# Performance work log

Measured on AMD Instinct MI355X. Metric: run time of the kernel, lower is better.

## Reference

```python
import jax, jax.numpy as jnp
import numpy as np

B, N, D, K = 32, 1024, 768, 512

def setup_inputs() -> dict:
    key = jax.random.key(0)
    k1, k2 = jax.random.split(key)
    img_feat_map = jax.random.normal(k1, (B, N, D), dtype=jnp.float32)
    codebook = jax.random.normal(k2, (K, D), dtype=jnp.float32)
    return {"img_feat_map": img_feat_map, "codebook": codebook}

def reference(img_feat_map, codebook):
    # squared L2 distances between each token and each codebook vector
    x_sq = jnp.sum(img_feat_map ** 2, axis=2, keepdims=True)          # [B,N,1]
    c_sq = jnp.sum(codebook ** 2, axis=1)[None, None, :]              # [1,1,K]
    dot = jnp.einsum('bnd,kd->bnk', img_feat_map, codebook)           # [B,N,K]
    distances = x_sq + c_sq - 2.0 * dot                               # [B,N,K]
    soft_assignments = jax.nn.softmax(-distances, axis=2)             # [B,N,K]
    # aggregate tokens per codebook slot
    aggregated = jnp.einsum('bnk,bnd->bkd', soft_assignments, img_feat_map)  # [B,K,D]
    return aggregated
```

## Files before the change

### kernel.cpp

```cpp
#include <hip/hip_runtime.h>
#include <math.h>

#define BB 32
#define NN 1024
#define DD 768
#define KK 512
#define MM (BB * NN)

typedef _Float16 half8 __attribute__((ext_vector_type(8)));
typedef _Float16 half4 __attribute__((ext_vector_type(4)));
typedef float floatx4 __attribute__((ext_vector_type(4)));

__device__ __forceinline__ void load_lds16(const void* g, void* l) {
    __builtin_amdgcn_global_load_lds(
        (const __attribute__((address_space(1))) unsigned int*)g,
        (__attribute__((address_space(3))) unsigned int*)l, 16, 0, 0);
}

__global__ __launch_bounds__(256) void prep_codebook(const float* __restrict__ cb,
                                                     _Float16* __restrict__ Cbh,
                                                     float* __restrict__ csq) {
    int k = blockIdx.x;
    const float* row = cb + (size_t)k * DD;
    _Float16* orow = Cbh + (size_t)k * DD;
    float s = 0.f;
    for (int d = threadIdx.x; d < DD; d += 256) {
        float v = row[d];
        s += v * v;
        orow[d] = (_Float16)v;
    }
    #pragma unroll
    for (int off = 32; off > 0; off >>= 1) s += __shfl_down(s, off);
    __shared__ float sm[4];
    int lane = threadIdx.x & 63, wid = threadIdx.x >> 6;
    if (lane == 0) sm[wid] = s;
    __syncthreads();
    if (threadIdx.x == 0) csq[k] = sm[0] + sm[1] + sm[2] + sm[3];
}

__global__ __launch_bounds__(512, 4) void fused_logits_softmax(
    const float* __restrict__ X,
    const _Float16* __restrict__ Cbh,
    const float* __restrict__ csq,
    _Float16* __restrict__ St,
    _Float16* __restrict__ Xt)
{
    __shared__ _Float16 Cs[2][512][32];
    __shared__ _Float16 Xs[2][64][32];
    __shared__ float redbuf[8][64];
    __shared__ float gred[64];

    const int t = threadIdx.x;
    const int w = t >> 6;
    const int lane = t & 63;
    const int l15 = lane & 15;
    const int quad = lane >> 4;
    const int wk = w * 64;
    const int gm0 = blockIdx.x * 64;
    const int b = gm0 >> 10;
    const int n0 = gm0 & 1023;

    const int qs = (quad ^ ((l15 >> 1) & 3)) * 8;

    float cs[4];
    #pragma unroll
    for (int ki = 0; ki < 4; ki++) cs[ki] = csq[wk + ki * 16 + l15];

    floatx4 acc[4][4] = {};

    const int cr = t >> 2;
    const int cq = (t & 3) ^ ((t >> 3) & 3);
    const float* xsrc = X + (size_t)(gm0 + cr) * DD + cq * 8;

    const int tdr = t >> 4;
    const int tn4 = (t & 15) * 4;

    float4 xa, xb;
    if (t < 256) { xa = *(const float4*)xsrc; xb = *(const float4*)(xsrc + 4); }

    #pragma unroll
    for (int c = 0; c < 4; c++)
        load_lds16(Cbh + (size_t)(c * 128 + cr) * DD + cq * 8,
                   (_Float16*)Cs[0] + (c * 512 + t) * 8);
    if (t < 256) {
        half8 h;
        h[0] = (_Float16)xa.x; h[1] = (_Float16)xa.y; h[2] = (_Float16)xa.z; h[3] = (_Float16)xa.w;
        h[4] = (_Float16)xb.x; h[5] = (_Float16)xb.y; h[6] = (_Float16)xb.z; h[7] = (_Float16)xb.w;
        *(half8*)&Xs[0][cr][(t & 3) * 8] = h;
        xa = *(const float4*)(xsrc + 32);
        xb = *(const float4*)(xsrc + 36);
    }
    __syncthreads();

    int cur = 0;
    for (int it = 0; it < 24; ++it) {
        const int d0 = it * 32;
        if (it + 1 < 24) {
            const int d0n = d0 + 32;
            #pragma unroll
            for (int c = 0; c < 4; c++)
                load_lds16(Cbh + (size_t)(c * 128 + cr) * DD + d0n + cq * 8,
                           (_Float16*)Cs[cur ^ 1] + (c * 512 + t) * 8);
            asm volatile("" ::: "memory");
            if (t < 256) {
                half8 h;
                h[0] = (_Float16)xa.x; h[1] = (_Float16)xa.y; h[2] = (_Float16)xa.z; h[3] = (_Float16)xa.w;
                h[4] = (_Float16)xb.x; h[5] = (_Float16)xb.y; h[6] = (_Float16)xb.z; h[7] = (_Float16)xb.w;
                *(half8*)&Xs[cur ^ 1][cr][(t & 3) * 8] = h;
                if (it + 2 < 24) {
                    xa = *(const float4*)(xsrc + (it + 2) * 32);
                    xb = *(const float4*)(xsrc + (it + 2) * 32 + 4);
                }
            }
        }
        {
            half4 xo;
            #pragma unroll
            for (int j = 0; j < 4; j++) {
                int n = tn4 + j;
                xo[j] = *((const _Float16*)Xs[cur] + n * 32 +
                          (((tdr >> 3) ^ ((n >> 1) & 3)) << 3) + (tdr & 7));
            }
            *(half4*)&Xt[((size_t)b * DD + d0 + tdr) * NN + n0 + tn4] = xo;
        }
        half8 af[4], bf[4];
        #pragma unroll
        for (int mi = 0; mi < 4; mi++)
            af[mi] = *(half8*)((_Float16*)Xs[cur] + (mi * 16 + l15) * 32 + qs);
        #pragma unroll
        for (int ki = 0; ki < 4; ki++)
            bf[ki] = *(half8*)((_Float16*)Cs[cur] + (wk + ki * 16 + l15) * 32 + qs);
        #pragma unroll
        for (int mi = 0; mi < 4; mi++)
            #pragma unroll
            for (int ki = 0; ki < 4; ki++)
                acc[mi][ki] = __builtin_amdgcn_mfma_f32_16x16x32_f16(af[mi], bf[ki], acc[mi][ki], 0, 0, 0);
        if (it + 1 < 24) {
            if (it + 2 < 24 && w < 4)
                asm volatile("s_waitcnt vmcnt(3) lgkmcnt(0)" ::: "memory");
            else
                asm volatile("s_waitcnt vmcnt(1) lgkmcnt(0)" ::: "memory");
            __builtin_amdgcn_s_barrier();
            cur ^= 1;
        }
    }

    float pmax[4][4];
    #pragma unroll
    for (int mi = 0; mi < 4; mi++)
        #pragma unroll
        for (int r = 0; r < 4; r++) {
            float m = -1e30f;
            #pragma unroll
            for (int ki = 0; ki < 4; ki++)
                m = fmaxf(m, 2.f * acc[mi][ki][r] - cs[ki]);
            pmax[mi][r] = m;
        }
    #pragma unroll
    for (int off = 1; off < 16; off <<= 1)
        #pragma unroll
        for (int mi = 0; mi < 4; mi++)
            #pragma unroll
            for (int r = 0; r < 4; r++)
                pmax[mi][r] = fmaxf(pmax[mi][r], __shfl_xor(pmax[mi][r], off));
    if (l15 == 0) {
        #pragma unroll
        for (int mi = 0; mi < 4; mi++)
            #pragma unroll
            for (int r = 0; r < 4; r++)
                redbuf[w][mi * 16 + quad * 4 + r] = pmax[mi][r];
    }
    __syncthreads();
    if (t < 64) {
        float g = redbuf[0][t];
        #pragma unroll
        for (int wv = 1; wv < 8; wv++) g = fmaxf(g, redbuf[wv][t]);
        gred[t] = g;
    }
    __syncthreads();
    float gmax[4][4];
    #pragma unroll
    for (int mi = 0; mi < 4; mi++)
        #pragma unroll
        for (int r = 0; r < 4; r++)
            gmax[mi][r] = gred[mi * 16 + quad * 4 + r];
    __syncthreads();

    float psum[4][4] = {};
    #pragma unroll
    for (int mi = 0; mi < 4; mi++)
        #pragma unroll
        for (int ki = 0; ki < 4; ki++) {
            floatx4 e;
            #pragma unroll
            for (int r = 0; r < 4; r++) {
                e[r] = __expf(2.f * acc[mi][ki][r] - cs[ki] - gmax[mi][r]);
                psum[mi][r] += e[r];
            }
            acc[mi][ki] = e;
        }
    #pragma unroll
    for (int off = 1; off < 16; off <<= 1)
        #pragma unroll
        for (int mi = 0; mi < 4; mi++)
            #pragma unroll
            for (int r = 0; r < 4; r++)
                psum[mi][r] += __shfl_xor(psum[mi][r], off);
    if (l15 == 0) {
        #pragma unroll
        for (int mi = 0; mi < 4; mi++)
            #pragma unroll
            for (int r = 0; r < 4; r++)
                redbuf[w][mi * 16 + quad * 4 + r] = psum[mi][r];
    }
    __syncthreads();
    if (t < 64) {
        float s = redbuf[0][t];
        #pragma unroll
        for (int wv = 1; wv < 8; wv++) s += redbuf[wv][t];
        gred[t] = 1.f / s;
    }
    __syncthreads();
    float ginv[4][4];
    #pragma unroll
    for (int mi = 0; mi < 4; mi++)
        #pragma unroll
        for (int r = 0; r < 4; r++)
            ginv[mi][r] = gred[mi * 16 + quad * 4 + r];

    #pragma unroll
    for (int mi = 0; mi < 4; mi++)
        #pragma unroll
        for (int ki = 0; ki < 4; ki++) {
            half4 s4;
            #pragma unroll
            for (int r = 0; r < 4; r++)
                s4[r] = (_Float16)(acc[mi][ki][r] * ginv[mi][r]);
            int k = wk + ki * 16 + l15;
            *(half4*)&St[((size_t)b * KK + k) * NN + n0 + mi * 16 + quad * 4] = s4;
        }
}

__global__ __launch_bounds__(256, 4) void gemm2_mfma(const _Float16* __restrict__ St,
                                                     const _Float16* __restrict__ Xt,
                                                     float* __restrict__ out) {
    __shared__ _Float16 As[2][128][32];
    __shared__ _Float16 Bs[2][128][32];

    const int lin = blockIdx.x;
    const int wg = (lin & 7) * 96 + (lin >> 3);
    const int b = wg / 24;
    const int rr = wg % 24;
    const int k0 = (rr / 6) * 128;
    const int d0 = (rr % 6) * 128;

    const int t = threadIdx.x;
    const int wave = t >> 6;
    const int lane = t & 63;
    const int wm = (wave >> 1) * 64;
    const int wn = (wave & 1) * 64;
    const int l15 = lane & 15;
    const int quad = lane >> 4;
    const int qs = (quad ^ ((l15 >> 1) & 3)) * 8;

    const int cr = t >> 2;
    const int cq = (t & 3) ^ ((t >> 3) & 3);

    floatx4 acc[4][4] = {};

    const _Float16* Abase = St + ((size_t)b * KK + k0) * NN;
    const _Float16* Bbase = Xt + ((size_t)b * DD + d0) * NN;

    #pragma unroll
    for (int c = 0; c < 2; c++) {
        load_lds16(Abase + (size_t)(c * 64 + cr) * NN + cq * 8,
                   (_Float16*)As[0] + (c * 256 + t) * 8);
        load_lds16(Bbase + (size_t)(c * 64 + cr) * NN + cq * 8,
                   (_Float16*)Bs[0] + (c * 256 + t) * 8);
    }
    __syncthreads();

    int cur = 0;
    for (int it = 0; it < 32; ++it) {
        if (it + 1 < 32) {
            const int n0 = (it + 1) * 32;
            #pragma unroll
            for (int c = 0; c < 2; c++) {
                load_lds16(Abase + (size_t)(c * 64 + cr) * NN + n0 + cq * 8,
                           (_Float16*)As[cur ^ 1] + (c * 256 + t) * 8);
                load_lds16(Bbase + (size_t)(c * 64 + cr) * NN + n0 + cq * 8,
                           (_Float16*)Bs[cur ^ 1] + (c * 256 + t) * 8);
            }
        }
        half8 af[4], bf[4];
        #pragma unroll
        for (int i = 0; i < 4; i++) af[i] = *(half8*)&As[cur][wm + i * 16 + l15][qs];
        #pragma unroll
        for (int i = 0; i < 4; i++) bf[i] = *(half8*)&Bs[cur][wn + i * 16 + l15][qs];
        #pragma unroll
        for (int mi = 0; mi < 4; mi++)
            #pragma unroll
            for (int ni = 0; ni < 4; ni++)
                acc[mi][ni] = __builtin_amdgcn_mfma_f32_16x16x32_f16(af[mi], bf[ni], acc[mi][ni], 0, 0, 0);
        if (it + 1 < 32) { __syncthreads(); cur ^= 1; }
    }

    #pragma unroll
    for (int ni = 0; ni < 4; ni++) {
        #pragma unroll
        for (int mi = 0; mi < 4; mi++) {
            int k = k0 + wm + mi * 16 + quad * 4;
            int d = d0 + wn + ni * 16 + l15;
            float* op = out + ((size_t)b * KK + k) * DD + d;
            floatx4 a = acc[mi][ni];
            op[0 * DD] = a[0];
            op[1 * DD] = a[1];
            op[2 * DD] = a[2];
            op[3 * DD] = a[3];
        }
    }
}

extern "C" void kernel_launch(void* const* d_in, const int* in_sizes, int n_in,
                              void* d_out, int out_size, void* d_ws, size_t ws_size,
                              hipStream_t stream) {
    const float* x  = (const float*)d_in[0];
    const float* cb = (const float*)d_in[1];
    float* out = (float*)d_out;

    char* ws = (char*)d_ws;
    float*    csq = (float*)ws;
    _Float16* Cbh = (_Float16*)(ws + 4096);
    _Float16* Xt  = (_Float16*)(ws + 4096 + 786432);
    _Float16* St  = (_Float16*)(ws + 4096 + 786432 + 50331648);

    prep_codebook<<<KK, 256, 0, stream>>>(cb, Cbh, csq);

    fused_logits_softmax<<<MM / 64, 512, 0, stream>>>(x, Cbh, csq, St, Xt);

    gemm2_mfma<<<768, 256, 0, stream>>>(St, Xt, out);
}
```

Before: 239.1 us.

## Triple-buffer LDS tiles and double fused-kernel waves to 1024 threads

Both GEMM-style kernels move from double to triple LDS buffering with a prefetch distance of two k-steps. Explicit vmcnt waits and raw s_barrier replace the full __syncthreads, to hide global-to-LDS latency. The fused logits/softmax kernel now runs 16 waves per block, each covering 32 codebook columns instead of 64. This cuts per-wave accumulator registers, but the larger LDS footprint (about 110KB) likely limits it to one block per CU, and the gemm2 launch bound drops to 3 blocks.

```diff
diff --git a/kernel.cpp b/kernel.cpp
--- a/kernel.cpp
+++ b/kernel.cpp
@@ -15,6 +15,15 @@
     __builtin_amdgcn_global_load_lds(
         (const __attribute__((address_space(1))) unsigned int*)g,
         (__attribute__((address_space(3))) unsigned int*)l, 16, 0, 0);
+}
+
+__device__ __forceinline__ void memfence() { asm volatile("" ::: "memory"); }
+
+__device__ __forceinline__ void cvt_store8(float4 a, float4 b, _Float16* dst) {
+    half8 h;
+    h[0] = (_Float16)a.x; h[1] = (_Float16)a.y; h[2] = (_Float16)a.z; h[3] = (_Float16)a.w;
+    h[4] = (_Float16)b.x; h[5] = (_Float16)b.y; h[6] = (_Float16)b.z; h[7] = (_Float16)b.w;
+    *(half8*)dst = h;
 }
 
 __global__ __launch_bounds__(256) void prep_codebook(const float* __restrict__ cb,
@@ -38,16 +47,16 @@
     if (threadIdx.x == 0) csq[k] = sm[0] + sm[1] + sm[2] + sm[3];
 }
 
-__global__ __launch_bounds__(512, 4) void fused_logits_softmax(
+__global__ __launch_bounds__(1024, 4) void fused_logits_softmax(
     const float* __restrict__ X,
     const _Float16* __restrict__ Cbh,
     const float* __restrict__ csq,
     _Float16* __restrict__ St,
     _Float16* __restrict__ Xt)
 {
-    __shared__ _Float16 Cs[2][512][32];
-    __shared__ _Float16 Xs[2][64][32];
-    __shared__ float redbuf[8][64];
+    __shared__ _Float16 Cs[3][512][32];
+    __shared__ _Float16 Xs[3][64][32];
+    __shared__ float redbuf[16][64];
     __shared__ float gred[64];
 
     const int t = threadIdx.x;
@@ -55,18 +64,18 @@
     const int lane = t & 63;
     const int l15 = lane & 15;
     const int quad = lane >> 4;
-    const int wk = w * 64;
+    const int wk = w * 32;
     const int gm0 = blockIdx.x * 64;
     const int b = gm0 >> 10;
     const int n0 = gm0 & 1023;
 
     const int qs = (quad ^ ((l15 >> 1) & 3)) * 8;
 
-    float cs[4];
-    #pragma unroll
-    for (int ki = 0; ki < 4; ki++) cs[ki] = csq[wk + ki * 16 + l15];
-
-    floatx4 acc[4][4] = {};
+    float cs[2];
+    #pragma unroll
+    for (int ki = 0; ki < 2; ki++) cs[ki] = csq[wk + ki * 16 + l15];
+
+    floatx4 acc[4][2] = {};
 
     const int cr = t >> 2;
     const int cq = (t & 3) ^ ((t >> 3) & 3);
@@ -75,45 +84,58 @@
     const int tdr = t >> 4;
     const int tn4 = (t & 15) * 4;
 
-    float4 xa, xb;
-    if (t < 256) { xa = *(const float4*)xsrc; xb = *(const float4*)(xsrc + 4); }
-
-    #pragma unroll
-    for (int c = 0; c < 4; c++)
-        load_lds16(Cbh + (size_t)(c * 128 + cr) * DD + cq * 8,
-                   (_Float16*)Cs[0] + (c * 512 + t) * 8);
+    float4 pca, pcb, pna, pnb;
     if (t < 256) {
-        half8 h;
-        h[0] = (_Float16)xa.x; h[1] = (_Float16)xa.y; h[2] = (_Float16)xa.z; h[3] = (_Float16)xa.w;
-        h[4] = (_Float16)xb.x; h[5] = (_Float16)xb.y; h[6] = (_Float16)xb.z; h[7] = (_Float16)xb.w;
-        *(half8*)&Xs[0][cr][(t & 3) * 8] = h;
-        xa = *(const float4*)(xsrc + 32);
-        xb = *(const float4*)(xsrc + 36);
-    }
-    __syncthreads();
+        float4 a0 = *(const float4*)xsrc;
+        float4 b0 = *(const float4*)(xsrc + 4);
+        float4 a1 = *(const float4*)(xsrc + 32);
+        float4 b1 = *(const float4*)(xsrc + 36);
+        cvt_store8(a0, b0, &Xs[0][cr][(t & 3) * 8]);
+        cvt_store8(a1, b1, &Xs[1][cr][(t & 3) * 8]);
+    }
+    #pragma unroll
+    for (int c = 0; c < 2; c++)
+        load_lds16(Cbh + (size_t)(c * 256 + cr) * DD + cq * 8,
+                   (_Float16*)Cs[0] + (c * 1024 + t) * 8);
+    memfence();
+    #pragma unroll
+    for (int c = 0; c < 2; c++)
+        load_lds16(Cbh + (size_t)(c * 256 + cr) * DD + 32 + cq * 8,
+                   (_Float16*)Cs[1] + (c * 1024 + t) * 8);
+    memfence();
+    if (t < 256) {
+        pca = *(const float4*)(xsrc + 64);
+        pcb = *(const float4*)(xsrc + 68);
+        pna = *(const float4*)(xsrc + 96);
+        pnb = *(const float4*)(xsrc + 100);
+    }
+    if (w < 4) asm volatile("s_waitcnt vmcnt(6) lgkmcnt(0)" ::: "memory");
+    else       asm volatile("s_waitcnt vmcnt(2) lgkmcnt(0)" ::: "memory");
+    __builtin_amdgcn_s_barrier();
 
     int cur = 0;
     for (int it = 0; it < 24; ++it) {
         const int d0 = it * 32;
-        if (it + 1 < 24) {
-            const int d0n = d0 + 32;
-            #pragma unroll
-            for (int c = 0; c < 4; c++)
-                load_lds16(Cbh + (size_t)(c * 128 + cr) * DD + d0n + cq * 8,
-                           (_Float16*)Cs[cur ^ 1] + (c * 512 + t) * 8);
-            asm volatile("" ::: "memory");
+        const int nxt = (cur == 2) ? 0 : cur + 1;
+        const int nx2 = (nxt == 2) ? 0 : nxt + 1;
+        if (it + 2 < 24) {
+            const int d0s = d0 + 64;
+            #pragma unroll
+            for (int c = 0; c < 2; c++)
+                load_lds16(Cbh + (size_t)(c * 256 + cr) * DD + d0s + cq * 8,
+                           (_Float16*)Cs[nx2] + (c * 1024 + t) * 8);
+            memfence();
             if (t < 256) {
-                half8 h;
-                h[0] = (_Float16)xa.x; h[1] = (_Float16)xa.y; h[2] = (_Float16)xa.z; h[3] = (_Float16)xa.w;
-                h[4] = (_Float16)xb.x; h[5] = (_Float16)xb.y; h[6] = (_Float16)xb.z; h[7] = (_Float16)xb.w;
-                *(half8*)&Xs[cur ^ 1][cr][(t & 3) * 8] = h;
-                if (it + 2 < 24) {
-                    xa = *(const float4*)(xsrc + (it + 2) * 32);
-                    xb = *(const float4*)(xsrc + (it + 2) * 32 + 4);
+                cvt_store8(pca, pcb, &Xs[nx2][cr][(t & 3) * 8]);
+                pca = pna; pcb = pnb;
+                if (it + 4 < 24) {
+                    pna = *(const float4*)(xsrc + (it + 4) * 32);
+                    pnb = *(const float4*)(xsrc + (it + 4) * 32 + 4);
                 }
-            }
-        }
-        {
+                memfence();
+            }
+        }
+        if (t < 512) {
             half4 xo;
             #pragma unroll
             for (int j = 0; j < 4; j++) {
@@ -123,25 +145,28 @@
             }
             *(half4*)&Xt[((size_t)b * DD + d0 + tdr) * NN + n0 + tn4] = xo;
         }
-        half8 af[4], bf[4];
+        half8 af[4], bf[2];
         #pragma unroll
         for (int mi = 0; mi < 4; mi++)
             af[mi] = *(half8*)((_Float16*)Xs[cur] + (mi * 16 + l15) * 32 + qs);
         #pragma unroll
-        for (int ki = 0; ki < 4; ki++)
+        for (int ki = 0; ki < 2; ki++)
             bf[ki] = *(half8*)((_Float16*)Cs[cur] + (wk + ki * 16 + l15) * 32 + qs);
         #pragma unroll
         for (int mi = 0; mi < 4; mi++)
             #pragma unroll
-            for (int ki = 0; ki < 4; ki++)
+            for (int ki = 0; ki < 2; ki++)
                 acc[mi][ki] = __builtin_amdgcn_mfma_f32_16x16x32_f16(af[mi], bf[ki], acc[mi][ki], 0, 0, 0);
         if (it + 1 < 24) {
-            if (it + 2 < 24 && w < 4)
-                asm volatile("s_waitcnt vmcnt(3) lgkmcnt(0)" ::: "memory");
-            else
-                asm volatile("s_waitcnt vmcnt(1) lgkmcnt(0)" ::: "memory");
+            if (it < 20) {
+                if (w < 4)      asm volatile("s_waitcnt vmcnt(5) lgkmcnt(0)" ::: "memory");
+                else if (w < 8) asm volatile("s_waitcnt vmcnt(3) lgkmcnt(0)" ::: "memory");
+                else            asm volatile("s_waitcnt vmcnt(2) lgkmcnt(0)" ::: "memory");
+            } else {
+                asm volatile("s_waitcnt vmcnt(0) lgkmcnt(0)" ::: "memory");
+            }
             __builtin_amdgcn_s_barrier();
-            cur ^= 1;
+            cur = nxt;
         }
     }
 
@@ -152,7 +177,7 @@
         for (int r = 0; r < 4; r++) {
             float m = -1e30f;
             #pragma unroll
-            for (int ki = 0; ki < 4; ki++)
+            for (int ki = 0; ki < 2; ki++)
                 m = fmaxf(m, 2.f * acc[mi][ki][r] - cs[ki]);
             pmax[mi][r] = m;
         }
@@ -174,7 +199,7 @@
     if (t < 64) {
         float g = redbuf[0][t];
         #pragma unroll
-        for (int wv = 1; wv < 8; wv++) g = fmaxf(g, redbuf[wv][t]);
+        for (int wv = 1; wv < 16; wv++) g = fmaxf(g, redbuf[wv][t]);
         gred[t] = g;
     }
     __syncthreads();
@@ -190,7 +215,7 @@
     #pragma unroll
     for (int mi = 0; mi < 4; mi++)
         #pragma unroll
-        for (int ki = 0; ki < 4; ki++) {
+        for (int ki = 0; ki < 2; ki++) {
             floatx4 e;
             #pragma unroll
             for (int r = 0; r < 4; r++) {
@@ -217,7 +242,7 @@
     if (t < 64) {
         float s = redbuf[0][t];
         #pragma unroll
-        for (int wv = 1; wv < 8; wv++) s += redbuf[wv][t];
+        for (int wv = 1; wv < 16; wv++) s += redbuf[wv][t];
         gred[t] = 1.f / s;
     }
     __syncthreads();
@@ -231,7 +256,7 @@
     #pragma unroll
     for (int mi = 0; mi < 4; mi++)
         #pragma unroll
-        for (int ki = 0; ki < 4; ki++) {
+        for (int ki = 0; ki < 2; ki++) {
             half4 s4;
             #pragma unroll
             for (int r = 0; r < 4; r++)
@@ -241,11 +266,11 @@
         }
 }
 
-__global__ __launch_bounds__(256, 4) void gemm2_mfma(const _Float16* __restrict__ St,
+__global__ __launch_bounds__(256, 3) void gemm2_mfma(const _Float16* __restrict__ St,
                                                      const _Float16* __restrict__ Xt,
                                                      float* __restrict__ out) {
-    __shared__ _Float16 As[2][128][32];
-    __shared__ _Float16 Bs[2][128][32];
+    __shared__ _Float16 As[3][128][32];
+    __shared__ _Float16 Bs[3][128][32];
 
     const int lin = blockIdx.x;
     const int wg = (lin & 7) * 96 + (lin >> 3);
@@ -278,31 +303,51 @@
         load_lds16(Bbase + (size_t)(c * 64 + cr) * NN + cq * 8,
                    (_Float16*)Bs[0] + (c * 256 + t) * 8);
     }
-    __syncthreads();
+    memfence();
+    #pragma unroll
+    for (int c = 0; c < 2; c++) {
+        load_lds16(Abase + (size_t)(c * 64 + cr) * NN + 32 + cq * 8,
+                   (_Float16*)As[1] + (c * 256 + t) * 8);
+        load_lds16(Bbase + (size_t)(c * 64 + cr) * NN + 32 + cq * 8,
+                   (_Float16*)Bs[1] + (c * 256 + t) * 8);
+    }
+    memfence();
+    asm volatile("s_waitcnt vmcnt(4)" ::: "memory");
+    __builtin_amdgcn_s_barrier();
 
     int cur = 0;
     for (int it = 0; it < 32; ++it) {
-        if (it + 1 < 32) {
-            const int n0 = (it + 1) * 32;
+        const int nxt = (cur == 2) ? 0 : cur + 1;
+        const int nx2 = (nxt == 2) ? 0 : nxt + 1;
+        if (it + 2 < 32) {
+            const int n0s = (it + 2) * 32;
             #pragma unroll
             for (int c = 0; c < 2; c++) {
-                load_lds16(Abase + (size_t)(c * 64 + cr) * NN + n0 + cq * 8,
-                           (_Float16*)As[cur ^ 1] + (c * 256 + t) * 8);
-                load_lds16(Bbase + (size_t)(c * 64 + cr) * NN + n0 + cq * 8,
-                           (_Float16*)Bs[cur ^ 1] + (c * 256 + t) * 8);
-            }
+                load_lds16(Abase + (size_t)(c * 64 + cr) * NN + n0s + cq * 8,
+                           (_Float16*)As[nx2] + (c * 256 + t) * 8);
+                load_lds16(Bbase + (size_t)(c * 64 + cr) * NN + n0s + cq * 8,
+                           (_Float16*)Bs[nx2] + (c * 256 + t) * 8);
+            }
+            memfence();
         }
         half8 af[4], bf[4];
         #pragma unroll
-        for (int i = 0; i < 4; i++) af[i] = *(half8*)&As[cur][wm + i * 16 + l15][qs];
-        #pragma unroll
-        for (int i = 0; i < 4; i++) bf[i] = *(half8*)&Bs[cur][wn + i * 16 + l15][qs];
+        for (int i = 0; i < 4; i++)
+            af[i] = *(half8*)((_Float16*)As[cur] + (wm + i * 16 + l15) * 32 + qs);
+        #pragma unroll
+        for (int i = 0; i < 4; i++)
+            bf[i] = *(half8*)((_Float16*)Bs[cur] + (wn + i * 16 + l15) * 32 + qs);
         #pragma unroll
         for (int mi = 0; mi < 4; mi++)
             #pragma unroll
             for (int ni = 0; ni < 4; ni++)
                 acc[mi][ni] = __builtin_amdgcn_mfma_f32_16x16x32_f16(af[mi], bf[ni], acc[mi][ni], 0, 0, 0);
-        if (it + 1 < 32) { __syncthreads(); cur ^= 1; }
+        if (it + 1 < 32) {
+            if (it < 30) asm volatile("s_waitcnt vmcnt(4) lgkmcnt(0)" ::: "memory");
+            else         asm volatile("s_waitcnt vmcnt(0) lgkmcnt(0)" ::: "memory");
+            __builtin_amdgcn_s_barrier();
+            cur = nxt;
+        }
     }
 
     #pragma unroll
@@ -336,7 +381,7 @@
 
     prep_codebook<<<KK, 256, 0, stream>>>(cb, Cbh, csq);
 
-    fused_logits_softmax<<<MM / 64, 512, 0, stream>>>(x, Cbh, csq, St, Xt);
+    fused_logits_softmax<<<MM / 64, 1024, 0, stream>>>(x, Cbh, csq, St, Xt);
 
     gemm2_mfma<<<768, 256, 0, stream>>>(St, Xt, out);
 }
```

Result: slower. 268.6 us (+12.4%).
